# Kernel optimization log

Hardware: AMD Instinct MI355X
Metric: run time of the kernel (lower is better)

## Reference

```python
import jax, jax.numpy as jnp
import numpy as np

N, E, D_IN, D_OUT = 50000, 800000, 128, 128


def setup_inputs() -> dict:
    key = jax.random.key(0)
    ks = jax.random.split(key, 4)
    x = jax.random.normal(ks[0], (N, D_IN), jnp.float32)
    edge_index = jax.random.randint(ks[1], (2, E), 0, N)
    # GCNConv.lin weight (no bias in lin; bias added after aggregation)
    W = jax.random.normal(ks[2], (D_IN, D_OUT), jnp.float32) / np.sqrt(D_IN)
    b = jnp.zeros((D_OUT,), jnp.float32)
    # edge_weight_predictor: Linear(2*dim_in, 1)
    w_pred = jax.random.normal(ks[3], (2 * D_IN, 1), jnp.float32) / np.sqrt(2 * D_IN)
    b_pred = jnp.zeros((1,), jnp.float32)
    return {"x": x, "edge_index": edge_index, "W": W, "b": b,
            "w_pred": w_pred, "b_pred": b_pred}


def reference(x, edge_index, W, b, w_pred, b_pred):
    n = x.shape[0]
    src, tgt = edge_index[0], edge_index[1]

    # --- learned edge weights: gather, concat, linear, sigmoid ---
    eemb = jnp.concatenate([x[src], x[tgt]], axis=1)          # [E, 2D]
    ew = jax.nn.sigmoid(eemb @ w_pred + b_pred)[:, 0]         # [E]

    # --- GCNConv with edge_weight (PyG gcn_norm: add self-loops w=1) ---
    loop = jnp.arange(n)
    row = jnp.concatenate([src, loop])                        # message sources
    col = jnp.concatenate([tgt, loop])                        # aggregation targets
    w_full = jnp.concatenate([ew, jnp.ones((n,), ew.dtype)])

    deg = jax.ops.segment_sum(w_full, col, num_segments=n)    # weighted in-degree
    dis = jnp.where(deg > 0, jax.lax.rsqrt(deg), 0.0)         # deg^{-1/2}, inf->0
    norm = dis[row] * w_full * dis[col]                       # [E+N]

    xw = x @ W                                                # [N, D_OUT]
    msg = norm[:, None] * xw[row]                             # [E+N, D_OUT]
    out = jax.ops.segment_sum(msg, col, num_segments=n) + b   # [N, D_OUT]
    return out
```

## Files before the change

kernel.cpp:

```cpp
#include <hip/hip_runtime.h>
#include <math.h>

#define D 128
#define GR 32
#define NC 16

__device__ __forceinline__ unsigned int bf16_round(float f) {
  unsigned int u = __float_as_uint(f);
  return (u + 0x7fffu + ((u >> 16) & 1u)) >> 16;
}
__device__ __forceinline__ float bf_lo(unsigned int u) { return __uint_as_float(u << 16); }
__device__ __forceinline__ float bf_hi(unsigned int u) { return __uint_as_float(u & 0xffff0000u); }

__global__ __launch_bounds__(256) void k_pq(const float* __restrict__ x,
                                            const float* __restrict__ w_pred,
                                            float* __restrict__ p, float* __restrict__ q,
                                            int n) {
  int wid = (blockIdx.x * blockDim.x + threadIdx.x) >> 6;
  int lane = threadIdx.x & 63;
  if (wid >= n) return;
  float2 xv = ((const float2*)(x + (size_t)wid * D))[lane];
  float2 wp = ((const float2*)w_pred)[lane];
  float2 wq = ((const float2*)w_pred)[64 + lane];
  float pp = xv.x * wp.x + xv.y * wp.y;
  float qq = xv.x * wq.x + xv.y * wq.y;
#pragma unroll
  for (int off = 32; off > 0; off >>= 1) {
    pp += __shfl_down(pp, off);
    qq += __shfl_down(qq, off);
  }
  if (lane == 0) { p[wid] = pp; q[wid] = qq; }
}

__global__ __launch_bounds__(256) void k_hist(const int* __restrict__ tgt,
                                              int* __restrict__ rank,
                                              int* __restrict__ partial,
                                              int E, int n) {
  int e = blockIdx.x * blockDim.x + threadIdx.x;
  if (e >= E) return;
  int t = tgt[e];
  int c = (e >> 8) & (NC - 1);
  rank[e] = atomicAdd(&partial[c * n + t], 1);
}

__global__ __launch_bounds__(256) void k_scan1(const int* __restrict__ partial,
                                               int* __restrict__ rowptr,
                                               int* __restrict__ bsum, int n) {
  __shared__ int wsum[4];
  int base = blockIdx.x * 1024 + threadIdx.x * 4;
  int4 v = make_int4(0, 0, 0, 0);
  if (base + 3 < n) {
#pragma unroll
    for (int c = 0; c < NC; ++c) {
      int4 t = *(const int4*)(partial + (size_t)c * n + base);
      v.x += t.x; v.y += t.y; v.z += t.z; v.w += t.w;
    }
  } else {
#pragma unroll
    for (int c = 0; c < NC; ++c) {
      const int* pc = partial + (size_t)c * n;
      if (base + 0 < n) v.x += pc[base + 0];
      if (base + 1 < n) v.y += pc[base + 1];
      if (base + 2 < n) v.z += pc[base + 2];
      if (base + 3 < n) v.w += pc[base + 3];
    }
  }
  int s = v.x + v.y + v.z + v.w;
  int lane = threadIdx.x & 63;
  int wave = threadIdx.x >> 6;
  int incl = s;
#pragma unroll
  for (int off = 1; off < 64; off <<= 1) {
    int t = __shfl_up(incl, off);
    if (lane >= off) incl += t;
  }
  if (lane == 63) wsum[wave] = incl;
  __syncthreads();
  int woff = 0;
#pragma unroll
  for (int w = 0; w < 4; ++w) if (w < wave) woff += wsum[w];
  int excl = woff + incl - s;
  if (base + 0 < n) rowptr[base + 0] = excl;
  if (base + 1 < n) rowptr[base + 1] = excl + v.x;
  if (base + 2 < n) rowptr[base + 2] = excl + v.x + v.y;
  if (base + 3 < n) rowptr[base + 3] = excl + v.x + v.y + v.z;
  if (threadIdx.x == 255) bsum[blockIdx.x] = woff + incl;
}

__global__ __launch_bounds__(256) void k_cursors(int* __restrict__ rowptr,
                                                 const int* __restrict__ bsum,
                                                 const int* __restrict__ partial,
                                                 int* __restrict__ cursor,
                                                 int n, int E, int nb) {
  __shared__ int bpre_s[64];
  if (threadIdx.x < 64) {
    int lane = threadIdx.x;
    int v = (lane < nb) ? bsum[lane] : 0;
    int incl = v;
#pragma unroll
    for (int off = 1; off < 64; off <<= 1) {
      int t = __shfl_up(incl, off);
      if (lane >= off) incl += t;
    }
    bpre_s[lane] = incl - v;
  }
  __syncthreads();
  int t = blockIdx.x * blockDim.x + threadIdx.x;
  if (t < n) {
    int r = rowptr[t] + bpre_s[t >> 10];
    rowptr[t] = r;
#pragma unroll
    for (int c = 0; c < NC; ++c) {
      cursor[c * n + t] = r;
      r += partial[c * n + t];
    }
  }
  if (t == 0) rowptr[n] = E;
}

__global__ __launch_bounds__(256) void k_fill(const int* __restrict__ src,
                                              const int* __restrict__ tgt,
                                              const int* __restrict__ rank,
                                              const int* __restrict__ cursor,
                                              int* __restrict__ ecol, int E, int n) {
  int e = blockIdx.x * blockDim.x + threadIdx.x;
  if (e >= E) return;
  int t = tgt[e];
  int c = (e >> 8) & (NC - 1);
  int pos = cursor[c * n + t] + rank[e];
  ecol[pos] = src[e];
}

__global__ __launch_bounds__(256) void k_node(const int* __restrict__ rowptr,
                                              const int* __restrict__ ecol,
                                              const float* __restrict__ p,
                                              const float* __restrict__ q,
                                              const float* __restrict__ b_pred,
                                              float* __restrict__ ewt,
                                              float* __restrict__ dis, int n) {
  int wid = (blockIdx.x * blockDim.x + threadIdx.x) >> 6;
  int lane = threadIdx.x & 63;
  if (wid >= n) return;
  int beg = rowptr[wid], end = rowptr[wid + 1];
  float qt = q[wid] + b_pred[0];
  float sum = 0.0f;
  for (int j0 = beg; j0 < end; j0 += 64) {
    int j = j0 + lane;
    float w = 0.0f;
    if (j < end) {
      int s = ecol[j];
      float z = p[s] + qt;
      w = 1.0f / (1.0f + expf(-z));
      ewt[j] = w;
    }
    sum += w;
  }
#pragma unroll
  for (int off = 32; off > 0; off >>= 1) sum += __shfl_down(sum, off);
  if (lane == 0) {
    float d = 1.0f + sum;
    dis[wid] = (d > 0.0f) ? rsqrtf(d) : 0.0f;
  }
}

__global__ __launch_bounds__(256) void k_gemm(const float* __restrict__ x,
                                              const float* __restrict__ W,
                                              const float* __restrict__ dis,
                                              unsigned int* __restrict__ xwh, int n) {
  __shared__ float Ws[64 * D];
  __shared__ float xs[GR * D];

  int row0 = blockIdx.x * GR;
  float4* xs4 = (float4*)xs;
  const float4* x4 = (const float4*)x;
  for (int i = threadIdx.x; i < GR * D / 4; i += 256) {
    int r = i >> 5;
    int gr = row0 + r;
    xs4[i] = (gr < n) ? x4[(size_t)gr * 32 + (i & 31)] : make_float4(0.f, 0.f, 0.f, 0.f);
  }

  int colg = threadIdx.x & 31;
  int rowg = threadIdx.x >> 5;
  float4 acc[4];
#pragma unroll
  for (int r = 0; r < 4; ++r) acc[r] = make_float4(0.f, 0.f, 0.f, 0.f);

  const float4* W4 = (const float4*)W;
  float4* Ws4 = (float4*)Ws;

  for (int half = 0; half < 2; ++half) {
    __syncthreads();
    for (int i = threadIdx.x; i < 64 * D / 4; i += 256)
      Ws4[i] = W4[half * (64 * D / 4) + i];
    __syncthreads();
#pragma unroll
    for (int k4 = 0; k4 < 16; ++k4) {
      float4 xv[4];
#pragma unroll
      for (int r = 0; r < 4; ++r)
        xv[r] = xs4[(rowg * 4 + r) * 32 + half * 16 + k4];
#pragma unroll
      for (int kk = 0; kk < 4; ++kk) {
        float4 w = Ws4[(k4 * 4 + kk) * 32 + colg];
#pragma unroll
        for (int r = 0; r < 4; ++r) {
          float xk = (&xv[r].x)[kk];
          acc[r].x = fmaf(xk, w.x, acc[r].x);
          acc[r].y = fmaf(xk, w.y, acc[r].y);
          acc[r].z = fmaf(xk, w.z, acc[r].z);
          acc[r].w = fmaf(xk, w.w, acc[r].w);
        }
      }
    }
  }

#pragma unroll
  for (int r = 0; r < 4; ++r) {
    int gr = row0 + rowg * 4 + r;
    if (gr < n) {
      float dv = dis[gr];
      uint2 pk;
      pk.x = bf16_round(acc[r].x * dv) | (bf16_round(acc[r].y * dv) << 16);
      pk.y = bf16_round(acc[r].z * dv) | (bf16_round(acc[r].w * dv) << 16);
      *(uint2*)(xwh + (size_t)gr * 64 + colg * 2) = pk;
    }
  }
}

__global__ __launch_bounds__(256) void k_gather(const int* __restrict__ rowptr,
                                                const int* __restrict__ ecol,
                                                const float* __restrict__ ewt,
                                                const uint4* __restrict__ xwh4,
                                                const float* __restrict__ dis,
                                                const float* __restrict__ b,
                                                float* __restrict__ out, int n) {
  int wid = (blockIdx.x * blockDim.x + threadIdx.x) >> 6;
  int lane = threadIdx.x & 63;
  if (wid >= n) return;
  int cj = lane & 15;
  int rg = lane >> 4;
  int beg = rowptr[wid], end = rowptr[wid + 1];

  float acc[8];
  if (rg == 0) {
    uint4 v = xwh4[(size_t)wid * 16 + cj];
    acc[0] = bf_lo(v.x); acc[1] = bf_hi(v.x);
    acc[2] = bf_lo(v.y); acc[3] = bf_hi(v.y);
    acc[4] = bf_lo(v.z); acc[5] = bf_hi(v.z);
    acc[6] = bf_lo(v.w); acc[7] = bf_hi(v.w);
  } else {
#pragma unroll
    for (int i = 0; i < 8; ++i) acc[i] = 0.0f;
  }

  for (int j0 = beg; j0 < end; j0 += 64) {
    int m = end - j0; if (m > 64) m = 64;
    int sl = 0; float cl = 0.0f;
    if (lane < m) { sl = ecol[j0 + lane]; cl = ewt[j0 + lane]; }
    for (int k = 0; k < m; k += 4) {
      int idx = k + rg;
      int s = __shfl(sl, idx);
      float c = __shfl(cl, idx);
      if (idx >= m) { s = 0; c = 0.0f; }
      uint4 v = xwh4[(size_t)s * 16 + cj];
      acc[0] = fmaf(c, bf_lo(v.x), acc[0]);
      acc[1] = fmaf(c, bf_hi(v.x), acc[1]);
      acc[2] = fmaf(c, bf_lo(v.y), acc[2]);
      acc[3] = fmaf(c, bf_hi(v.y), acc[3]);
      acc[4] = fmaf(c, bf_lo(v.z), acc[4]);
      acc[5] = fmaf(c, bf_hi(v.z), acc[5]);
      acc[6] = fmaf(c, bf_lo(v.w), acc[6]);
      acc[7] = fmaf(c, bf_hi(v.w), acc[7]);
    }
  }

#pragma unroll
  for (int i = 0; i < 8; ++i) {
    acc[i] += __shfl_xor(acc[i], 16);
    acc[i] += __shfl_xor(acc[i], 32);
  }

  if (rg == 0) {
    float dt = dis[wid];
    float4 b0 = ((const float4*)b)[cj * 2];
    float4 b1 = ((const float4*)b)[cj * 2 + 1];
    float4 o0, o1;
    o0.x = fmaf(dt, acc[0], b0.x); o0.y = fmaf(dt, acc[1], b0.y);
    o0.z = fmaf(dt, acc[2], b0.z); o0.w = fmaf(dt, acc[3], b0.w);
    o1.x = fmaf(dt, acc[4], b1.x); o1.y = fmaf(dt, acc[5], b1.y);
    o1.z = fmaf(dt, acc[6], b1.z); o1.w = fmaf(dt, acc[7], b1.w);
    ((float4*)out)[(size_t)wid * 32 + cj * 2] = o0;
    ((float4*)out)[(size_t)wid * 32 + cj * 2 + 1] = o1;
  }
}

extern "C" void kernel_launch(void* const* d_in, const int* in_sizes, int n_in,
                              void* d_out, int out_size, void* d_ws, size_t ws_size,
                              hipStream_t stream) {
  const float* x      = (const float*)d_in[0];
  const int*   ei     = (const int*)d_in[1];
  const float* W      = (const float*)d_in[2];
  const float* b      = (const float*)d_in[3];
  const float* w_pred = (const float*)d_in[4];
  const float* b_pred = (const float*)d_in[5];

  int n = in_sizes[0] / D;
  int E = in_sizes[1] / 2;
  const int* src = ei;
  const int* tgt = ei + E;

  float* out = (float*)d_out;
  float* ws  = (float*)d_ws;
  unsigned int* xwh = (unsigned int*)ws;
  float* p       = ws + (size_t)n * 64;
  float* q       = p + n;
  float* dis     = q + n;
  float* ewt     = dis + n;
  int*   ecol    = (int*)(ewt + E);
  int*   rank    = ecol + E;
  int*   partial = rank + E;
  int*   cursor  = partial + (size_t)NC * n;
  int*   rowptr  = cursor + (size_t)NC * n;
  int*   bsum    = rowptr + n + 1;

  int nb = (n + 1023) / 1024;

  (void)hipMemsetAsync(partial, 0, (size_t)NC * n * sizeof(int), stream);
  k_pq<<<(n + 3) / 4, 256, 0, stream>>>(x, w_pred, p, q, n);
  k_hist<<<(E + 255) / 256, 256, 0, stream>>>(tgt, rank, partial, E, n);
  k_scan1<<<nb, 256, 0, stream>>>(partial, rowptr, bsum, n);
  k_cursors<<<(n + 255) / 256, 256, 0, stream>>>(rowptr, bsum, partial, cursor, n, E, nb);
  k_fill<<<(E + 255) / 256, 256, 0, stream>>>(src, tgt, rank, cursor, ecol, E, n);
  k_node<<<(n + 3) / 4, 256, 0, stream>>>(rowptr, ecol, p, q, b_pred, ewt, dis, n);
  k_gemm<<<(n + GR - 1) / GR, 256, 0, stream>>>(x, W, dis, xwh, n);
  k_gather<<<(n + 3) / 4, 256, 0, stream>>>(rowptr, ecol, ewt, (const uint4*)xwh, dis, b, out, n);
}
```

Baseline: 224.3 us.

## Replace FP32 SIMT GEMM with bf16 MFMA using pre-converted x and transposed W

The k_pq kernel now also writes a bf16 copy of x, and a new small kernel writes a transposed bf16 copy of W. The dense x@W GEMM now runs on the matrix cores with mfma_f32_16x16x32_bf16: each wave computes 16 rows by 128 columns, stages the result in shared memory, then scales by dis and packs it to bf16. This removes the FP32 FMA-bound shared-memory GEMM. In exchange it adds an extra bf16 write of x, one extra launch, and lower input precision in the GEMM.

```diff
diff --git a/kernel.cpp b/kernel.cpp
--- a/kernel.cpp
+++ b/kernel.cpp
@@ -2,8 +2,10 @@
 #include <math.h>
 
 #define D 128
-#define GR 32
 #define NC 16
+
+typedef __attribute__((ext_vector_type(8))) short bf16x8;
+typedef __attribute__((ext_vector_type(4))) float f32x4;
 
 __device__ __forceinline__ unsigned int bf16_round(float f) {
   unsigned int u = __float_as_uint(f);
@@ -15,11 +17,12 @@
 __global__ __launch_bounds__(256) void k_pq(const float* __restrict__ x,
                                             const float* __restrict__ w_pred,
                                             float* __restrict__ p, float* __restrict__ q,
-                                            int n) {
+                                            unsigned int* __restrict__ xbh, int n) {
   int wid = (blockIdx.x * blockDim.x + threadIdx.x) >> 6;
   int lane = threadIdx.x & 63;
   if (wid >= n) return;
   float2 xv = ((const float2*)(x + (size_t)wid * D))[lane];
+  xbh[(size_t)wid * 64 + lane] = bf16_round(xv.x) | (bf16_round(xv.y) << 16);
   float2 wp = ((const float2*)w_pred)[lane];
   float2 wq = ((const float2*)w_pred)[64 + lane];
   float pp = xv.x * wp.x + xv.y * wp.y;
@@ -30,6 +33,13 @@
     qq += __shfl_down(qq, off);
   }
   if (lane == 0) { p[wid] = pp; q[wid] = qq; }
+}
+
+__global__ __launch_bounds__(256) void k_wt(const float* __restrict__ W,
+                                            unsigned short* __restrict__ wt) {
+  int i = blockIdx.x * 256 + threadIdx.x;
+  int col = i >> 7, k = i & 127;
+  wt[col * 128 + k] = (unsigned short)bf16_round(W[k * 128 + col]);
 }
 
 __global__ __launch_bounds__(256) void k_hist(const int* __restrict__ tgt,
@@ -163,66 +173,61 @@
   }
 }
 
-__global__ __launch_bounds__(256) void k_gemm(const float* __restrict__ x,
-                                              const float* __restrict__ W,
-                                              const float* __restrict__ dis,
-                                              unsigned int* __restrict__ xwh, int n) {
-  __shared__ float Ws[64 * D];
-  __shared__ float xs[GR * D];
-
-  int row0 = blockIdx.x * GR;
-  float4* xs4 = (float4*)xs;
-  const float4* x4 = (const float4*)x;
-  for (int i = threadIdx.x; i < GR * D / 4; i += 256) {
-    int r = i >> 5;
-    int gr = row0 + r;
-    xs4[i] = (gr < n) ? x4[(size_t)gr * 32 + (i & 31)] : make_float4(0.f, 0.f, 0.f, 0.f);
-  }
-
-  int colg = threadIdx.x & 31;
-  int rowg = threadIdx.x >> 5;
-  float4 acc[4];
-#pragma unroll
-  for (int r = 0; r < 4; ++r) acc[r] = make_float4(0.f, 0.f, 0.f, 0.f);
-
-  const float4* W4 = (const float4*)W;
-  float4* Ws4 = (float4*)Ws;
-
-  for (int half = 0; half < 2; ++half) {
-    __syncthreads();
-    for (int i = threadIdx.x; i < 64 * D / 4; i += 256)
-      Ws4[i] = W4[half * (64 * D / 4) + i];
-    __syncthreads();
-#pragma unroll
-    for (int k4 = 0; k4 < 16; ++k4) {
-      float4 xv[4];
-#pragma unroll
-      for (int r = 0; r < 4; ++r)
-        xv[r] = xs4[(rowg * 4 + r) * 32 + half * 16 + k4];
-#pragma unroll
-      for (int kk = 0; kk < 4; ++kk) {
-        float4 w = Ws4[(k4 * 4 + kk) * 32 + colg];
-#pragma unroll
-        for (int r = 0; r < 4; ++r) {
-          float xk = (&xv[r].x)[kk];
-          acc[r].x = fmaf(xk, w.x, acc[r].x);
-          acc[r].y = fmaf(xk, w.y, acc[r].y);
-          acc[r].z = fmaf(xk, w.z, acc[r].z);
-          acc[r].w = fmaf(xk, w.w, acc[r].w);
-        }
-      }
-    }
-  }
-
-#pragma unroll
-  for (int r = 0; r < 4; ++r) {
-    int gr = row0 + rowg * 4 + r;
-    if (gr < n) {
-      float dv = dis[gr];
-      uint2 pk;
-      pk.x = bf16_round(acc[r].x * dv) | (bf16_round(acc[r].y * dv) << 16);
-      pk.y = bf16_round(acc[r].z * dv) | (bf16_round(acc[r].w * dv) << 16);
-      *(uint2*)(xwh + (size_t)gr * 64 + colg * 2) = pk;
+__global__ __launch_bounds__(256) void k_gemm_mfma(const short* __restrict__ xbh,
+                                                   const short* __restrict__ wt,
+                                                   const float* __restrict__ dis,
+                                                   unsigned int* __restrict__ xwh, int n) {
+  __shared__ float cbuf[4][16 * 128];
+  int wave = threadIdx.x >> 6;
+  int lane = threadIdx.x & 63;
+  int row0 = blockIdx.x * 64 + wave * 16;
+  int rA = lane & 15, quad = lane >> 4;
+
+  f32x4 acc[8];
+#pragma unroll
+  for (int cb = 0; cb < 8; ++cb) acc[cb] = (f32x4){0.f, 0.f, 0.f, 0.f};
+
+  const short* arow = xbh + (size_t)(row0 + rA) * 128 + quad * 8;
+  bool arow_ok = (row0 + rA) < n;
+#pragma unroll
+  for (int kk = 0; kk < 4; ++kk) {
+    bf16x8 a;
+    if (arow_ok) a = *(const bf16x8*)(arow + kk * 32);
+    else a = (bf16x8){0, 0, 0, 0, 0, 0, 0, 0};
+#pragma unroll
+    for (int cb = 0; cb < 8; ++cb) {
+      bf16x8 bf = *(const bf16x8*)(wt + (size_t)(cb * 16 + rA) * 128 + kk * 32 + quad * 8);
+      acc[cb] = __builtin_amdgcn_mfma_f32_16x16x32_bf16(a, bf, acc[cb], 0, 0, 0);
+    }
+  }
+
+#pragma unroll
+  for (int cb = 0; cb < 8; ++cb)
+#pragma unroll
+    for (int r = 0; r < 4; ++r)
+      cbuf[wave][(quad * 4 + r) * 128 + cb * 16 + rA] = acc[cb][r];
+  __syncthreads();
+
+  int rr = lane >> 2;
+  int ch = (lane & 3) * 32;
+  int grow = row0 + rr;
+  if (grow < n) {
+    float dv = dis[grow];
+    const float* cr = &cbuf[wave][rr * 128 + ch];
+#pragma unroll
+    for (int g = 0; g < 2; ++g) {
+      uint4 o;
+      o.x = bf16_round(cr[g * 16 + 0] * dv)  | (bf16_round(cr[g * 16 + 1] * dv) << 16);
+      o.y = bf16_round(cr[g * 16 + 2] * dv)  | (bf16_round(cr[g * 16 + 3] * dv) << 16);
+      o.z = bf16_round(cr[g * 16 + 4] * dv)  | (bf16_round(cr[g * 16 + 5] * dv) << 16);
+      o.w = bf16_round(cr[g * 16 + 6] * dv)  | (bf16_round(cr[g * 16 + 7] * dv) << 16);
+      uint4 o2;
+      o2.x = bf16_round(cr[g * 16 + 8] * dv)  | (bf16_round(cr[g * 16 + 9] * dv) << 16);
+      o2.y = bf16_round(cr[g * 16 + 10] * dv) | (bf16_round(cr[g * 16 + 11] * dv) << 16);
+      o2.z = bf16_round(cr[g * 16 + 12] * dv) | (bf16_round(cr[g * 16 + 13] * dv) << 16);
+      o2.w = bf16_round(cr[g * 16 + 14] * dv) | (bf16_round(cr[g * 16 + 15] * dv) << 16);
+      *(uint4*)(xwh + (size_t)grow * 64 + (ch >> 1) + g * 8)     = o;
+      *(uint4*)(xwh + (size_t)grow * 64 + (ch >> 1) + g * 8 + 4) = o2;
     }
   }
 }
@@ -312,7 +317,8 @@
   float* out = (float*)d_out;
   float* ws  = (float*)d_ws;
   unsigned int* xwh = (unsigned int*)ws;
-  float* p       = ws + (size_t)n * 64;
+  unsigned int* xbh = xwh + (size_t)n * 64;
+  float* p       = (float*)(xbh + (size_t)n * 64);
   float* q       = p + n;
   float* dis     = q + n;
   float* ewt     = dis + n;
@@ -322,16 +328,18 @@
   int*   cursor  = partial + (size_t)NC * n;
   int*   rowptr  = cursor + (size_t)NC * n;
   int*   bsum    = rowptr + n + 1;
+  unsigned short* wt = (unsigned short*)(bsum + 64);
 
   int nb = (n + 1023) / 1024;
 
   (void)hipMemsetAsync(partial, 0, (size_t)NC * n * sizeof(int), stream);
-  k_pq<<<(n + 3) / 4, 256, 0, stream>>>(x, w_pred, p, q, n);
+  k_pq<<<(n + 3) / 4, 256, 0, stream>>>(x, w_pred, p, q, xbh, n);
+  k_wt<<<64, 256, 0, stream>>>(W, wt);
   k_hist<<<(E + 255) / 256, 256, 0, stream>>>(tgt, rank, partial, E, n);
   k_scan1<<<nb, 256, 0, stream>>>(partial, rowptr, bsum, n);
   k_cursors<<<(n + 255) / 256, 256, 0, stream>>>(rowptr, bsum, partial, cursor, n, E, nb);
   k_fill<<<(E + 255) / 256, 256, 0, stream>>>(src, tgt, rank, cursor, ecol, E, n);
   k_node<<<(n + 3) / 4, 256, 0, stream>>>(rowptr, ecol, p, q, b_pred, ewt, dis, n);
-  k_gemm<<<(n + GR - 1) / GR, 256, 0, stream>>>(x, W, dis, xwh, n);
+  k_gemm_mfma<<<(n + 63) / 64, 256, 0, stream>>>((const short*)xbh, (const short*)wt, dis, xwh, n);
   k_gather<<<(n + 3) / 4, 256, 0, stream>>>(rowptr, ecol, ewt, (const uint4*)xwh, dis, b, out, n);
 }
```

After: 213.7 us. 4.7% less time.
